# Optimization experiments

Measured on AMD Instinct MI355X. Metric: run time of the kernel, lower is better.

Reference implementation:

```python
import jax, jax.numpy as jnp
import numpy as np

N_NODES = 200000
N_EDGES = 6400000
F_OUT = 128
N_GRAPHS = 64


def setup_inputs() -> dict:
    key = jax.random.key(0)
    ks = jax.random.split(key, 6)
    x = jax.random.normal(ks[0], (N_NODES, 1), dtype=jnp.float32)
    edge_index = jax.random.randint(ks[1], (2, N_EDGES), 0, N_NODES, dtype=jnp.int64)
    batch = jnp.sort(jax.random.randint(ks[2], (N_NODES,), 0, N_GRAPHS, dtype=jnp.int64))
    edge_weights = jax.random.uniform(ks[3], (N_EDGES,), dtype=jnp.float32)
    W_l = jax.random.normal(ks[4], (F_OUT, 1), dtype=jnp.float32)
    b_l = jnp.zeros((F_OUT,), dtype=jnp.float32)
    W_r = jax.random.normal(ks[5], (F_OUT, 1), dtype=jnp.float32)
    return {"x": x, "edge_index": edge_index, "batch": batch,
            "edge_weights": edge_weights, "W_l": W_l, "b_l": b_l, "W_r": W_r}


def reference(x, edge_index, batch, edge_weights, W_l, b_l, W_r):
    # SAGEConv (mean aggregation, edge-weighted messages as in PyG propagate):
    #   out_i = lin_l( mean_{j in N(i)} w_ij * x_j ) + lin_r(x_i)
    n = x.shape[0]
    src, dst = edge_index[0], edge_index[1]
    msgs = x[src] * edge_weights[:, None]                      # [E, 1] gather
    agg_sum = jax.ops.segment_sum(msgs, dst, num_segments=n)  # [N, 1] scatter-add
    deg = jax.ops.segment_sum(jnp.ones((src.shape[0],), x.dtype), dst, num_segments=n)
    agg = agg_sum / jnp.maximum(deg, 1.0)[:, None]             # mean
    h = agg @ W_l.T + b_l + x @ W_r.T                          # [N, F_OUT]
    # dropout(p=0.2) is identity in eval mode -> omitted
    out = jax.ops.segment_max(h, batch, num_segments=N_GRAPHS)  # global_max_pool
    return out
```

## Files before the change

### kernel.cpp

```cpp
#include <hip/hip_runtime.h>
#include <hip/hip_bf16.h>
#include <float.h>
#include <math.h>

constexpr int NN = 200000;
constexpr int NE = 6400000;
constexpr int FO = 128;
constexpr int NG = 64;

constexpr int NCHUNK = 512;
constexpr int CHUNK  = NE / NCHUNK;
constexpr int C4     = CHUNK / 4;
constexpr int BNODES = 1024;
constexpr int NBUK   = (NN + BNODES - 1) / BNODES;

constexpr float Q_SCALE = 4096.0f;
constexpr float Q_INV   = 1.0f / 4096.0f;

__device__ __forceinline__ unsigned encf(float f) {
    unsigned u = __float_as_uint(f);
    return (u & 0x80000000u) ? ~u : (u | 0x80000000u);
}
__device__ __forceinline__ float decf(unsigned e) {
    unsigned u = (e & 0x80000000u) ? (e & 0x7FFFFFFFu) : ~e;
    return __uint_as_float(u);
}

__device__ __forceinline__ unsigned short q16(float m) {
    int q = __float2int_rn(m * Q_SCALE) + 32768;
    return (unsigned short)min(max(q, 0), 65535);
}

__global__ __launch_bounds__(1024) void k_histmsg(const int* __restrict__ ei,
                       const float* __restrict__ x, const float* __restrict__ w,
                       unsigned* __restrict__ cnt, unsigned short* __restrict__ msg,
                       unsigned* __restrict__ out_enc,
                       const int* __restrict__ batch, int* __restrict__ start) {
    __shared__ unsigned h[NBUK];
    int c = blockIdx.x, tid = threadIdx.x;
    for (int i = tid; i < NBUK; i += 1024) h[i] = 0u;
    if (c == 0) for (int i = tid; i < NG * FO; i += 1024) out_enc[i] = encf(-INFINITY);
    if (c == 1 && tid <= NG) {
        if (tid == NG) start[tid] = NN;
        else {
            int lo = 0, hi = NN;
            while (lo < hi) { int mid = (lo + hi) >> 1; if (batch[mid] < tid) lo = mid + 1; else hi = mid; }
            start[tid] = lo;
        }
    }
    __syncthreads();
    const int4*   s4 = (const int4*)(ei + c * CHUNK);
    const int4*   d4 = (const int4*)(ei + NE + c * CHUNK);
    const float4* w4 = (const float4*)(w + c * CHUNK);
    ushort4*      m4 = (ushort4*)(msg + c * CHUNK);
#pragma unroll
    for (int k = 0; k < 4; ++k) {
        int idx = tid + k * 1024;
        if (idx >= C4) continue;
        int4 dv = d4[idx];
        atomicAdd(&h[dv.x >> 10], 1u);
        atomicAdd(&h[dv.y >> 10], 1u);
        atomicAdd(&h[dv.z >> 10], 1u);
        atomicAdd(&h[dv.w >> 10], 1u);
        int4   sv = s4[idx];
        float4 wv = w4[idx];
        ushort4 mq;
        mq.x = q16(x[sv.x] * wv.x);
        mq.y = q16(x[sv.y] * wv.y);
        mq.z = q16(x[sv.z] * wv.z);
        mq.w = q16(x[sv.w] * wv.w);
        m4[idx] = mq;
    }
    __syncthreads();
    for (int i = tid; i < NBUK; i += 1024) cnt[i * NCHUNK + c] = h[i];
}

__global__ __launch_bounds__(NCHUNK) void k_scanA(unsigned* __restrict__ cnt, unsigned* __restrict__ T) {
    __shared__ unsigned s[NCHUNK];
    int b = blockIdx.x, t = threadIdx.x;
    unsigned v = cnt[b * NCHUNK + t];
    s[t] = v;
    __syncthreads();
    for (int off = 1; off < NCHUNK; off <<= 1) {
        unsigned u = (t >= off) ? s[t - off] : 0u;
        __syncthreads();
        s[t] += u;
        __syncthreads();
    }
    cnt[b * NCHUNK + t] = s[t] - v;
    if (t == NCHUNK - 1) T[b] = s[t];
}

__global__ void k_scanB(const unsigned* __restrict__ T, unsigned* __restrict__ B) {
    __shared__ unsigned s[256];
    int t = threadIdx.x;
    unsigned v = (t < NBUK) ? T[t] : 0u;
    s[t] = v;
    __syncthreads();
    for (int off = 1; off < 256; off <<= 1) {
        unsigned u = (t >= off) ? s[t - off] : 0u;
        __syncthreads();
        s[t] += u;
        __syncthreads();
    }
    if (t < NBUK) B[t] = s[t] - v;
    if (t == 255) B[NBUK] = s[255];
}

__global__ __launch_bounds__(1024) void k_sort(const int* __restrict__ ei,
                        const unsigned short* __restrict__ msg,
                        const unsigned* __restrict__ cnt,
                        const unsigned* __restrict__ T,
                        const unsigned* __restrict__ B,
                        unsigned* __restrict__ rec,
                        int blo, int bhi, unsigned cap) {
    __shared__ unsigned lincl[256];
    __shared__ unsigned loffs[NBUK];
    __shared__ unsigned gbase[NBUK];
    __shared__ unsigned recbuf[CHUNK];
    int c = blockIdx.x, tid = threadIdx.x;
    int nb = bhi - blo;

    unsigned sz = 0;
    if (tid < nb) {
        int b = blo + tid;
        unsigned pre = cnt[b * NCHUNK + c];
        unsigned nxt = (c + 1 < NCHUNK) ? cnt[b * NCHUNK + c + 1] : T[b];
        sz = nxt - pre;
        gbase[b] = B[b] - B[blo] + pre;
    }
    if (tid < 256) lincl[tid] = sz;
    __syncthreads();
    for (int off = 1; off < 256; off <<= 1) {
        unsigned v = 0;
        if (tid < 256 && tid >= off) v = lincl[tid - off];
        __syncthreads();
        if (tid < 256) lincl[tid] += v;
        __syncthreads();
    }
    if (tid < nb) loffs[blo + tid] = lincl[tid] - sz;
    __syncthreads();

    const int4*    d4 = (const int4*)(ei + NE + c * CHUNK);
    const ushort4* m4 = (const ushort4*)(msg + c * CHUNK);
#pragma unroll
    for (int k = 0; k < 4; ++k) {
        int idx = tid + k * 1024;
        if (idx >= C4) continue;
        int4    dv = d4[idx];
        ushort4 mv = m4[idx];
        int      ds_[4] = {dv.x, dv.y, dv.z, dv.w};
        unsigned mq[4]  = {mv.x, mv.y, mv.z, mv.w};
#pragma unroll
        for (int j = 0; j < 4; ++j) {
            int d = ds_[j], b = d >> 10;
            if (b < blo || b >= bhi) continue;
            unsigned ls = atomicAdd(&loffs[b], 1u);
            recbuf[ls] = ((unsigned)(d & (BNODES - 1)) << 16) | mq[j];
        }
    }
    __syncthreads();

    int wave = tid >> 6, lane = tid & 63;
    for (int lb = wave; lb < nb; lb += 16) {
        unsigned s0 = lb ? lincl[lb - 1] : 0u;
        unsigned s1 = lincl[lb];
        unsigned g0 = gbase[blo + lb];
        for (unsigned i = s0 + lane; i < s1; i += 64) {
            unsigned g = g0 + (i - s0);
            if (g < cap) rec[g] = recbuf[i];
        }
    }
}

__global__ __launch_bounds__(1024) void k_bucket(const unsigned* __restrict__ rec,
                         const unsigned* __restrict__ B,
                         float* __restrict__ mean, int blo) {
    __shared__ unsigned long long acc[BNODES];
    int b = blo + blockIdx.x, tid = threadIdx.x;
    for (int i = tid; i < BNODES; i += 1024) acc[i] = 0ull;
    __syncthreads();
    unsigned b0 = B[blo];
    unsigned r0 = B[b] - b0, r1 = B[b + 1] - b0;
    for (unsigned r = r0 + tid; r < r1; r += 1024) {
        unsigned v = rec[r];
        atomicAdd(&acc[v >> 16], (1ull << 48) | (unsigned long long)(v & 0xFFFFu));
    }
    __syncthreads();
    int n0 = b * BNODES;
    for (int i = tid; i < BNODES; i += 1024) {
        int n = n0 + i;
        if (n < NN) {
            unsigned long long a = acc[i];
            float cn = (float)(unsigned)(a >> 48);
            float sq = (float)(a & 0xFFFFFFFFFFFFull);
            float sum = (sq - 32768.0f * cn) * Q_INV;
            mean[n] = sum / fmaxf(cn, 1.0f);
        }
    }
}

constexpr int SPLITS = 16;
__global__ void k_max8(const float* __restrict__ mean, const float* __restrict__ x,
                       const float* __restrict__ Wl, const float* __restrict__ Wr,
                       const int* __restrict__ start, unsigned* __restrict__ out_enc) {
    int g = blockIdx.x;
    int lo = start[g], hi = start[g + 1];
    int len = hi - lo;
    if (len <= 0) return;
    int per = (len + gridDim.y - 1) / gridDim.y;
    int a0 = lo + blockIdx.y * per;
    int a1 = min(a0 + per, hi);
    if (a0 >= a1) return;
    int f = threadIdx.x;
    float wl = Wl[f], wr = Wr[f];
    float m0 = -INFINITY, m1 = -INFINITY;
    int i = a0;
    for (; i + 2 <= a1; i += 2) {
        m0 = fmaxf(m0, fmaf(mean[i],     wl, x[i]     * wr));
        m1 = fmaxf(m1, fmaf(mean[i + 1], wl, x[i + 1] * wr));
    }
    if (i < a1) m0 = fmaxf(m0, fmaf(mean[i], wl, x[i] * wr));
    atomicMax(&out_enc[g * FO + f], encf(fmaxf(m0, m1)));
}

__global__ void k_decode(const unsigned* __restrict__ out_enc,
                         const float* __restrict__ bl, float* __restrict__ out) {
    int i = blockIdx.x * blockDim.x + threadIdx.x;
    if (i >= NG * FO) return;
    out[i] = decf(out_enc[i]) + bl[i & (FO - 1)];
}

constexpr float FP_SCALE = 16777216.0f;
constexpr float FP_INV   = 1.0f / FP_SCALE;
__device__ __forceinline__ unsigned long long pack_msg(float m) {
    return (1ull << 48) + (unsigned long long)(__float2ll_rn(m * FP_SCALE) + (1ll << 30));
}
__global__ void k_init1(unsigned long long* __restrict__ agg, unsigned* __restrict__ out_enc,
                        const int* __restrict__ batch, int* __restrict__ start) {
    int i = blockIdx.x * blockDim.x + threadIdx.x;
    if (i < NN) agg[i] = 0ull;
    if (i < NG * FO) out_enc[i] = encf(-INFINITY);
    if (i <= NG) {
        if (i == NG) start[i] = NN;
        else {
            int lo = 0, hi = NN;
            while (lo < hi) { int mid = (lo + hi) >> 1; if (batch[mid] < i) lo = mid + 1; else hi = mid; }
            start[i] = lo;
        }
    }
}
__global__ void k_scatter1(const int* __restrict__ ei, const float* __restrict__ x,
                           const float* __restrict__ w, unsigned long long* __restrict__ agg) {
    int t = blockIdx.x * blockDim.x + threadIdx.x;
    int e0 = t * 4;
    if (e0 >= NE) return;
    int4 sv = *(const int4*)(ei + e0);
    int4 dv = *(const int4*)(ei + NE + e0);
    float4 wv = *(const float4*)(w + e0);
    atomicAdd(&agg[dv.x], pack_msg(x[sv.x] * wv.x));
    atomicAdd(&agg[dv.y], pack_msg(x[sv.y] * wv.y));
    atomicAdd(&agg[dv.z], pack_msg(x[sv.z] * wv.z));
    atomicAdd(&agg[dv.w], pack_msg(x[sv.w] * wv.w));
}
__global__ void k_max1(const unsigned long long* __restrict__ agg, const float* __restrict__ x,
                       const float* __restrict__ Wl, const float* __restrict__ Wr,
                       const int* __restrict__ start, unsigned* __restrict__ out_enc) {
    int g = blockIdx.x;
    int lo = start[g], hi = start[g + 1];
    if (hi - lo <= 0) return;
    int per = (hi - lo + gridDim.y - 1) / gridDim.y;
    int a0 = lo + blockIdx.y * per, a1 = min(a0 + per, hi);
    if (a0 >= a1) return;
    int f = threadIdx.x;
    float wl = Wl[f], wr = Wr[f], m = -INFINITY;
    for (int i = a0; i < a1; ++i) {
        unsigned long long v = agg[i];
        int cnt = (int)(v >> 48);
        long long sfp = (long long)(v & 0xFFFFFFFFFFFFull) - ((long long)cnt << 30);
        float av = ((float)sfp * FP_INV) / fmaxf((float)cnt, 1.0f);
        m = fmaxf(m, fmaf(av, wl, x[i] * wr));
    }
    atomicMax(&out_enc[g * FO + f], encf(m));
}

extern "C" void kernel_launch(void* const* d_in, const int* in_sizes, int n_in,
                              void* d_out, int out_size, void* d_ws, size_t ws_size,
                              hipStream_t stream) {
    const float* x  = (const float*)d_in[0];
    const int*   ei = (const int*)d_in[1];
    const int*   bt = (const int*)d_in[2];
    const float* ew = (const float*)d_in[3];
    const float* Wl = (const float*)d_in[4];
    const float* bl = (const float*)d_in[5];
    const float* Wr = (const float*)d_in[6];
    float* out = (float*)d_out;
    char* ws = (char*)d_ws;

    const size_t MSG_B = (size_t)NE * 2;
    const size_t FIXED = (size_t)NBUK * NCHUNK * 4
                       + 1024
                       + 1024
                       + 800000
                       + 32768
                       + 512
                       + 256;
    int nphase = 0;
    unsigned cap = 0;
    for (int p = 1; p <= 3; ++p) {
        unsigned c = (unsigned)(NE / p) + 16384u;
        if (ws_size >= FIXED + MSG_B + (size_t)c * 4) { nphase = p; cap = c; break; }
    }

    if (nphase) {
        size_t off = 0;
        unsigned* rec  = (unsigned*)(ws + off); off += (size_t)cap * 4;           off = (off + 15) & ~15ull;
        unsigned short* msg = (unsigned short*)(ws + off); off += MSG_B;          off = (off + 15) & ~15ull;
        unsigned* cnt  = (unsigned*)(ws + off); off += (size_t)NBUK * NCHUNK * 4; off = (off + 15) & ~15ull;
        unsigned* T    = (unsigned*)(ws + off); off += 1024;
        unsigned* B    = (unsigned*)(ws + off); off += 1024;
        float*    mean = (float*)(ws + off);    off += 800000;                    off = (off + 15) & ~15ull;
        unsigned* out_enc = (unsigned*)(ws + off); off += 32768;
        int*      start   = (int*)(ws + off);

        k_histmsg<<<NCHUNK, 1024, 0, stream>>>(ei, x, ew, cnt, msg, out_enc, bt, start);
        k_scanA<<<NBUK, NCHUNK, 0, stream>>>(cnt, T);
        k_scanB<<<1, 256, 0, stream>>>(T, B);
        int per = (NBUK + nphase - 1) / nphase;
        for (int p = 0; p < nphase; ++p) {
            int blo = p * per;
            int bhi = min(blo + per, NBUK);
            if (blo >= bhi) break;
            k_sort<<<NCHUNK, 1024, 0, stream>>>(ei, msg, cnt, T, B, rec, blo, bhi, cap);
            k_bucket<<<bhi - blo, 1024, 0, stream>>>(rec, B, mean, blo);
        }
        k_max8<<<dim3(NG, SPLITS), FO, 0, stream>>>(mean, x, Wl, Wr, start, out_enc);
        k_decode<<<(NG * FO + 255) / 256, 256, 0, stream>>>(out_enc, bl, out);
    } else {
        unsigned long long* agg = (unsigned long long*)ws;
        unsigned* out_enc = (unsigned*)(ws + 1600000);
        int*      start   = (int*)(ws + 1600000 + 32768);
        k_init1<<<(NN + 255) / 256, 256, 0, stream>>>(agg, out_enc, bt, start);
        k_scatter1<<<(NE / 4 + 255) / 256, 256, 0, stream>>>(ei, x, ew, agg);
        k_max1<<<dim3(NG, 32), FO, 0, stream>>>(agg, x, Wl, Wr, start, out_enc);
        k_decode<<<(NG * FO + 255) / 256, 256, 0, stream>>>(out_enc, bl, out);
    }
}
```

Baseline: 82.56 us.

## Replace per-bucket scan with atomic global offsets and drop multi-phase sort

```diff
diff --git a/kernel.cpp b/kernel.cpp
--- a/kernel.cpp
+++ b/kernel.cpp
@@ -25,15 +25,15 @@
     unsigned u = (e & 0x80000000u) ? (e & 0x7FFFFFFFu) : ~e;
     return __uint_as_float(u);
 }
-
 __device__ __forceinline__ unsigned short q16(float m) {
     int q = __float2int_rn(m * Q_SCALE) + 32768;
     return (unsigned short)min(max(q, 0), 65535);
 }
 
-__global__ __launch_bounds__(1024) void k_histmsg(const int* __restrict__ ei,
+__global__ __launch_bounds__(1024) void k_histmsg2(const int* __restrict__ ei,
                        const float* __restrict__ x, const float* __restrict__ w,
-                       unsigned* __restrict__ cnt, unsigned short* __restrict__ msg,
+                       unsigned short* __restrict__ msg,
+                       unsigned* __restrict__ gcount, unsigned* __restrict__ cpack,
                        unsigned* __restrict__ out_enc,
                        const int* __restrict__ batch, int* __restrict__ start) {
     __shared__ unsigned h[NBUK];
@@ -72,29 +72,17 @@
         m4[idx] = mq;
     }
     __syncthreads();
-    for (int i = tid; i < NBUK; i += 1024) cnt[i * NCHUNK + c] = h[i];
-}
-
-__global__ __launch_bounds__(NCHUNK) void k_scanA(unsigned* __restrict__ cnt, unsigned* __restrict__ T) {
-    __shared__ unsigned s[NCHUNK];
-    int b = blockIdx.x, t = threadIdx.x;
-    unsigned v = cnt[b * NCHUNK + t];
-    s[t] = v;
-    __syncthreads();
-    for (int off = 1; off < NCHUNK; off <<= 1) {
-        unsigned u = (t >= off) ? s[t - off] : 0u;
-        __syncthreads();
-        s[t] += u;
-        __syncthreads();
-    }
-    cnt[b * NCHUNK + t] = s[t] - v;
-    if (t == NCHUNK - 1) T[b] = s[t];
-}
-
-__global__ void k_scanB(const unsigned* __restrict__ T, unsigned* __restrict__ B) {
+    for (int i = tid; i < NBUK; i += 1024) {
+        unsigned sz = h[i];
+        unsigned gpos = sz ? atomicAdd(&gcount[i], sz) : 0u;
+        cpack[i * NCHUNK + c] = (gpos << 14) | sz;
+    }
+}
+
+__global__ void k_scanB2(const unsigned* __restrict__ gcount, unsigned* __restrict__ B) {
     __shared__ unsigned s[256];
     int t = threadIdx.x;
-    unsigned v = (t < NBUK) ? T[t] : 0u;
+    unsigned v = (t < NBUK) ? gcount[t] : 0u;
     s[t] = v;
     __syncthreads();
     for (int off = 1; off < 256; off <<= 1) {
@@ -107,27 +95,22 @@
     if (t == 255) B[NBUK] = s[255];
 }
 
-__global__ __launch_bounds__(1024) void k_sort(const int* __restrict__ ei,
+__global__ __launch_bounds__(1024) void k_sortR(const int* __restrict__ ei,
                         const unsigned short* __restrict__ msg,
-                        const unsigned* __restrict__ cnt,
-                        const unsigned* __restrict__ T,
+                        const unsigned* __restrict__ cpack,
                         const unsigned* __restrict__ B,
-                        unsigned* __restrict__ rec,
-                        int blo, int bhi, unsigned cap) {
+                        unsigned* __restrict__ rec) {
     __shared__ unsigned lincl[256];
     __shared__ unsigned loffs[NBUK];
     __shared__ unsigned gbase[NBUK];
     __shared__ unsigned recbuf[CHUNK];
     int c = blockIdx.x, tid = threadIdx.x;
-    int nb = bhi - blo;
 
     unsigned sz = 0;
-    if (tid < nb) {
-        int b = blo + tid;
-        unsigned pre = cnt[b * NCHUNK + c];
-        unsigned nxt = (c + 1 < NCHUNK) ? cnt[b * NCHUNK + c + 1] : T[b];
-        sz = nxt - pre;
-        gbase[b] = B[b] - B[blo] + pre;
+    if (tid < NBUK) {
+        unsigned pk = cpack[tid * NCHUNK + c];
+        sz = pk & 0x3FFFu;
+        gbase[tid] = B[tid] + (pk >> 14);
     }
     if (tid < 256) lincl[tid] = sz;
     __syncthreads();
@@ -138,7 +121,7 @@
         if (tid < 256) lincl[tid] += v;
         __syncthreads();
     }
-    if (tid < nb) loffs[blo + tid] = lincl[tid] - sz;
+    if (tid < NBUK) loffs[tid] = lincl[tid] - sz;
     __syncthreads();
 
     const int4*    d4 = (const int4*)(ei + NE + c * CHUNK);
@@ -153,35 +136,33 @@
         unsigned mq[4]  = {mv.x, mv.y, mv.z, mv.w};
 #pragma unroll
         for (int j = 0; j < 4; ++j) {
-            int d = ds_[j], b = d >> 10;
-            if (b < blo || b >= bhi) continue;
-            unsigned ls = atomicAdd(&loffs[b], 1u);
+            int d = ds_[j];
+            unsigned ls = atomicAdd(&loffs[d >> 10], 1u);
             recbuf[ls] = ((unsigned)(d & (BNODES - 1)) << 16) | mq[j];
         }
     }
     __syncthreads();
 
     int wave = tid >> 6, lane = tid & 63;
-    for (int lb = wave; lb < nb; lb += 16) {
+    for (int lb = wave; lb < NBUK; lb += 16) {
         unsigned s0 = lb ? lincl[lb - 1] : 0u;
         unsigned s1 = lincl[lb];
-        unsigned g0 = gbase[blo + lb];
+        unsigned gb = gbase[lb];
         for (unsigned i = s0 + lane; i < s1; i += 64) {
-            unsigned g = g0 + (i - s0);
-            if (g < cap) rec[g] = recbuf[i];
+            unsigned g = gb + (i - s0);
+            if (g < (unsigned)NE) rec[g] = recbuf[i];
         }
     }
 }
 
 __global__ __launch_bounds__(1024) void k_bucket(const unsigned* __restrict__ rec,
                          const unsigned* __restrict__ B,
-                         float* __restrict__ mean, int blo) {
+                         float* __restrict__ mean) {
     __shared__ unsigned long long acc[BNODES];
-    int b = blo + blockIdx.x, tid = threadIdx.x;
+    int b = blockIdx.x, tid = threadIdx.x;
     for (int i = tid; i < BNODES; i += 1024) acc[i] = 0ull;
     __syncthreads();
-    unsigned b0 = B[blo];
-    unsigned r0 = B[b] - b0, r1 = B[b + 1] - b0;
+    unsigned r0 = B[b], r1 = B[b + 1];
     for (unsigned r = r0 + tid; r < r1; r += 1024) {
         unsigned v = rec[r];
         atomicAdd(&acc[v >> 16], (1ull << 48) | (unsigned long long)(v & 0xFFFFu));
@@ -297,43 +278,30 @@
     float* out = (float*)d_out;
     char* ws = (char*)d_ws;
 
-    const size_t MSG_B = (size_t)NE * 2;
-    const size_t FIXED = (size_t)NBUK * NCHUNK * 4
-                       + 1024
-                       + 1024
-                       + 800000
-                       + 32768
-                       + 512
-                       + 256;
-    int nphase = 0;
-    unsigned cap = 0;
-    for (int p = 1; p <= 3; ++p) {
-        unsigned c = (unsigned)(NE / p) + 16384u;
-        if (ws_size >= FIXED + MSG_B + (size_t)c * 4) { nphase = p; cap = c; break; }
-    }
-
-    if (nphase) {
+    const size_t REC_B  = (size_t)NE * 4;
+    const size_t MSG_B  = (size_t)NE * 2;
+    const size_t CPK_B  = (size_t)NBUK * NCHUNK * 4;
+    const size_t NEED   = REC_B + MSG_B + CPK_B
+                        + 1024 + 1024
+                        + 800000
+                        + 32768 + 512 + 256;
+
+    if (ws_size >= NEED) {
         size_t off = 0;
-        unsigned* rec  = (unsigned*)(ws + off); off += (size_t)cap * 4;           off = (off + 15) & ~15ull;
-        unsigned short* msg = (unsigned short*)(ws + off); off += MSG_B;          off = (off + 15) & ~15ull;
-        unsigned* cnt  = (unsigned*)(ws + off); off += (size_t)NBUK * NCHUNK * 4; off = (off + 15) & ~15ull;
-        unsigned* T    = (unsigned*)(ws + off); off += 1024;
-        unsigned* B    = (unsigned*)(ws + off); off += 1024;
-        float*    mean = (float*)(ws + off);    off += 800000;                    off = (off + 15) & ~15ull;
-        unsigned* out_enc = (unsigned*)(ws + off); off += 32768;
-        int*      start   = (int*)(ws + off);
-
-        k_histmsg<<<NCHUNK, 1024, 0, stream>>>(ei, x, ew, cnt, msg, out_enc, bt, start);
-        k_scanA<<<NBUK, NCHUNK, 0, stream>>>(cnt, T);
-        k_scanB<<<1, 256, 0, stream>>>(T, B);
-        int per = (NBUK + nphase - 1) / nphase;
-        for (int p = 0; p < nphase; ++p) {
-            int blo = p * per;
-            int bhi = min(blo + per, NBUK);
-            if (blo >= bhi) break;
-            k_sort<<<NCHUNK, 1024, 0, stream>>>(ei, msg, cnt, T, B, rec, blo, bhi, cap);
-            k_bucket<<<bhi - blo, 1024, 0, stream>>>(rec, B, mean, blo);
-        }
+        unsigned*       rec   = (unsigned*)(ws + off);       off += REC_B;
+        unsigned short* msg   = (unsigned short*)(ws + off); off += MSG_B;  off = (off + 15) & ~15ull;
+        unsigned*       cpack = (unsigned*)(ws + off);       off += CPK_B;
+        unsigned*       gcount = (unsigned*)(ws + off);      off += 1024;
+        unsigned*       B     = (unsigned*)(ws + off);       off += 1024;
+        float*          mean  = (float*)(ws + off);          off += 800000; off = (off + 15) & ~15ull;
+        unsigned*       out_enc = (unsigned*)(ws + off);     off += 32768;
+        int*            start   = (int*)(ws + off);
+
+        hipMemsetAsync(gcount, 0, NBUK * sizeof(unsigned), stream);
+        k_histmsg2<<<NCHUNK, 1024, 0, stream>>>(ei, x, ew, msg, gcount, cpack, out_enc, bt, start);
+        k_scanB2<<<1, 256, 0, stream>>>(gcount, B);
+        k_sortR<<<NCHUNK, 1024, 0, stream>>>(ei, msg, cpack, B, rec);
+        k_bucket<<<NBUK, 1024, 0, stream>>>(rec, B, mean);
         k_max8<<<dim3(NG, SPLITS), FO, 0, stream>>>(mean, x, Wl, Wr, start, out_enc);
         k_decode<<<(NG * FO + 255) / 256, 256, 0, stream>>>(out_enc, bl, out);
     } else {
```

Result: slower. 88.85 us (+7.6%).
